# Kernel optimization log

Hardware: AMD Instinct MI355X
Metric: run time of the kernel (lower is better)

Reference implementation:

```python
import jax, jax.numpy as jnp
import numpy as np

D = 1024
H = 16
HD = D // H
S = 2048
B = 2
INNER = 4 * D
EPS = 1e-5


def _layernorm(x, w, b):
    mu = jnp.mean(x, axis=-1, keepdims=True)
    var = jnp.mean(jnp.square(x - mu), axis=-1, keepdims=True)
    return (x - mu) * jax.lax.rsqrt(var + EPS) * w + b


def _rope(x, cos, sin):
    # x: [B, S, H, HD]; cos/sin: [S, HD//2]
    xe, xo = x[..., 0::2], x[..., 1::2]
    c = cos[None, :, None, :]
    s = sin[None, :, None, :]
    oe = xe * c - xo * s
    oo = xe * s + xo * c
    return jnp.stack([oe, oo], axis=-1).reshape(x.shape)


def setup_inputs() -> dict:
    key = jax.random.key(0)
    ks = jax.random.split(key, 12)
    hidden_states = jax.random.normal(ks[0], (B, S, D), dtype=jnp.float32)
    time_step_emb = jax.random.normal(ks[1], (B, 6 * D), dtype=jnp.float32)
    # causal additive mask [1,1,S,S]
    causal = jnp.tril(jnp.ones((S, S), dtype=bool))
    attention_mask = jnp.where(causal, 0.0, -1e9).astype(jnp.float32)[None, None]
    # proper RoPE tables
    inv_freq = 1.0 / (10000.0 ** (np.arange(0, HD, 2, dtype=np.float32) / HD))
    t = np.arange(S, dtype=np.float32)
    freqs = np.outer(t, inv_freq)  # [S, HD//2]
    rope_cos = jnp.asarray(np.cos(freqs))
    rope_sin = jnp.asarray(np.sin(freqs))
    p = 0.02
    params = dict(
        ln1_w=jnp.ones((D,), jnp.float32), ln1_b=jnp.zeros((D,), jnp.float32),
        ln2_w=jnp.ones((D,), jnp.float32), ln2_b=jnp.zeros((D,), jnp.float32),
        c_attn_w=jax.random.normal(ks[2], (D, 3 * D), jnp.float32) * p,
        c_attn_b=jnp.zeros((3 * D,), jnp.float32),
        c_proj_w=jax.random.normal(ks[3], (D, D), jnp.float32) * p,
        c_proj_b=jnp.zeros((D,), jnp.float32),
        fc_w=jax.random.normal(ks[4], (D, INNER), jnp.float32) * p,
        fc_b=jnp.zeros((INNER,), jnp.float32),
        proj_w=jax.random.normal(ks[5], (INNER, D), jnp.float32) * p,
        proj_b=jnp.zeros((D,), jnp.float32),
        scale_shift_table=jax.random.normal(ks[6], (6, D), jnp.float32) / np.sqrt(D),
    )
    return dict(hidden_states=hidden_states, attention_mask=attention_mask,
                time_step_emb=time_step_emb, rope_cos=rope_cos, rope_sin=rope_sin,
                **params)


def reference(hidden_states, attention_mask, time_step_emb, rope_cos, rope_sin,
              ln1_w, ln1_b, ln2_w, ln2_b, c_attn_w, c_attn_b, c_proj_w, c_proj_b,
              fc_w, fc_b, proj_w, proj_b, scale_shift_table):
    b = hidden_states.shape[0]
    mods = scale_shift_table[None] + time_step_emb.reshape(b, 6, D)  # [B,6,D]
    sh_msa, sc_msa, g_msa, sh_mlp, sc_mlp, g_mlp = [mods[:, i:i + 1] for i in range(6)]

    residual = hidden_states
    h = _layernorm(hidden_states, ln1_w, ln1_b) * (1.0 + sc_msa) + sh_msa

    qkv = h @ c_attn_w + c_attn_b  # [B,S,3D]
    q, k, v = jnp.split(qkv, 3, axis=-1)
    q = _rope(q.reshape(b, S, H, HD), rope_cos, rope_sin)
    k = _rope(k.reshape(b, S, H, HD), rope_cos, rope_sin)
    v = v.reshape(b, S, H, HD)
    scores = jnp.einsum('bqhd,bkhd->bhqk', q, k) / np.sqrt(float(HD))
    scores = scores + attention_mask
    attn = jax.nn.softmax(scores, axis=-1)
    out = jnp.einsum('bhqk,bkhd->bqhd', attn, v).reshape(b, S, D)
    attn_out = out @ c_proj_w + c_proj_b

    hidden = attn_out * g_msa + residual
    residual = hidden
    h = _layernorm(hidden, ln2_w, ln2_b) * (1.0 + sc_mlp) + sh_mlp
    h = jax.nn.gelu(h @ fc_w + fc_b, approximate=True)  # gelu_new (tanh approx)
    h = h @ proj_w + proj_b
    return h * g_mlp + residual
```

## Files before the change

### kernel.cpp

```cpp
#include <hip/hip_runtime.h>
#include <hip/hip_bf16.h>

#define D_MODEL 1024
#define N_HEADS 16
#define HEAD_DIM 64
#define SEQ 2048
#define BATCH 2
#define INNER_DIM 4096
#define ROWS (BATCH*SEQ)

using f32x4  = __attribute__((ext_vector_type(4))) float;
using bf16x8 = __attribute__((ext_vector_type(8))) short;

__device__ __forceinline__ void gl_lds16(const void* g, void* l) {
  __builtin_amdgcn_global_load_lds(
      (const __attribute__((address_space(1))) void*)g,
      (__attribute__((address_space(3))) void*)l, 16, 0, 0);
}

__device__ __forceinline__ float bf2f(unsigned short u) {
  union { unsigned int i; float f; } v; v.i = ((unsigned int)u) << 16; return v.f;
}
__device__ __forceinline__ unsigned short f2bf(float f) {
  union { float f; unsigned int i; } v; v.f = f;
  unsigned int x = v.i;
  return (unsigned short)((x + 0x7fffu + ((x >> 16) & 1u)) >> 16);
}

__device__ __forceinline__ float exp2fast(float x) {
  return __builtin_amdgcn_exp2f(x);
}

__device__ __forceinline__ float gelu_tanh(float x) {
  float x3 = x * x * x;
  float z = 0.7978845608028654f * (x + 0.044715f * x3);
  z = fminf(z, 15.0f);
  float e = __expf(2.0f * z);
  float th = (e - 1.0f) / (e + 1.0f);
  return 0.5f * x * (1.0f + th);
}

__global__ void transpose_convert(const float* __restrict__ in,
                                  unsigned short* __restrict__ out,
                                  int K, int N) {
  __shared__ float tile[32][33];
  int n0 = blockIdx.x * 32, k0 = blockIdx.y * 32;
  int tx = threadIdx.x, ty = threadIdx.y;
#pragma unroll
  for (int i = 0; i < 4; i++)
    tile[ty + i * 8][tx] = in[(size_t)(k0 + ty + i * 8) * N + n0 + tx];
  __syncthreads();
#pragma unroll
  for (int i = 0; i < 4; i++)
    out[(size_t)(n0 + ty + i * 8) * K + k0 + tx] = f2bf(tile[tx][ty + i * 8]);
}

template<int SH_IDX, int SC_IDX>
__global__ void ln_mod_kernel(const float* __restrict__ x,
                              const float* __restrict__ lw,
                              const float* __restrict__ lb,
                              const float* __restrict__ sst,
                              const float* __restrict__ temb,
                              unsigned short* __restrict__ out) {
  int row = blockIdx.x;
  int b = row >> 11;
  int t = threadIdx.x;
  const float* xr = x + (size_t)row * D_MODEL;
  float4 v = ((const float4*)xr)[t];
  float s = v.x + v.y + v.z + v.w;
  float s2 = v.x * v.x + v.y * v.y + v.z * v.z + v.w * v.w;
#pragma unroll
  for (int o = 1; o < 64; o <<= 1) { s += __shfl_xor(s, o); s2 += __shfl_xor(s2, o); }
  __shared__ float red[8];
  int wid = t >> 6, lane = t & 63;
  if (lane == 0) { red[wid] = s; red[4 + wid] = s2; }
  __syncthreads();
  s = red[0] + red[1] + red[2] + red[3];
  s2 = red[4] + red[5] + red[6] + red[7];
  float mu = s * (1.0f / D_MODEL);
  float var = s2 * (1.0f / D_MODEL) - mu * mu;
  float rs = rsqrtf(var + 1e-5f);
  int d0 = t * 4;
  float xv[4] = { v.x, v.y, v.z, v.w };
  ushort4 ov;
  unsigned short* po = (unsigned short*)&ov;
#pragma unroll
  for (int j = 0; j < 4; j++) {
    int d = d0 + j;
    float ln = (xv[j] - mu) * rs * lw[d] + lb[d];
    float sc = sst[SC_IDX * D_MODEL + d] + temb[b * 6 * D_MODEL + SC_IDX * D_MODEL + d];
    float sh = sst[SH_IDX * D_MODEL + d] + temb[b * 6 * D_MODEL + SH_IDX * D_MODEL + d];
    po[j] = f2bf(ln * (1.0f + sc) + sh);
  }
  *((ushort4*)(out + (size_t)row * D_MODEL + d0)) = ov;
}

enum { EPI_QKV = 0, EPI_GELU = 2, EPI_PART = 3 };

template<int EPI>
__global__ __launch_bounds__(256, 2)
void gemm64(const unsigned short* __restrict__ A,
            const unsigned short* __restrict__ Bt,
            const float* __restrict__ bias,
            void* C0, void* C1,
            int N, int Ksub, int Kstride,
            const float* __restrict__ cosb,
            const float* __restrict__ sinb) {
  __shared__ unsigned short Alds[2][128 * 64];
  __shared__ unsigned short Blds[2][128 * 64];
  const int t = threadIdx.x;
  const int w = t >> 6, l = t & 63;
  const int lg = l >> 4, ll = l & 15;
  const int wm = w >> 1, wn = w & 1;
  const int kbase = blockIdx.z * Ksub;

  const int nx = gridDim.x;
  const int nwg = nx * gridDim.y;
  const int lid = blockIdx.y * nx + blockIdx.x;
  const int nid = (lid & 7) * (nwg >> 3) + (lid >> 3);
  const int m0 = (nid / nx) * 128, n0 = (nid % nx) * 128;

  void* Cout = blockIdx.z ? C1 : C0;

  f32x4 acc[4][4] = {};

  auto stage = [&](int kt, int buf) {
#pragma unroll
    for (int i = 0; i < 4; i++) {
      int c = i * 256 + t;
      int row = c >> 3, q = c & 7;
      gl_lds16(A + (size_t)(m0 + row) * Kstride + kbase + kt * 64 + ((q ^ (row & 7)) << 3),
               (char*)&Alds[buf][0] + c * 16);
    }
#pragma unroll
    for (int i = 0; i < 4; i++) {
      int c = i * 256 + t;
      int row = c >> 3, q = c & 7;
      gl_lds16(Bt + (size_t)(n0 + row) * Kstride + kbase + kt * 64 + ((q ^ (row & 7)) << 3),
               (char*)&Blds[buf][0] + c * 16);
    }
  };

  stage(0, 0);
  int buf = 0;
  const int nk = Ksub >> 6;
  for (int it = 0; it < nk; ++it) {
    if (it + 1 < nk) {
      stage(it + 1, buf ^ 1);
      asm volatile("s_waitcnt vmcnt(8)" ::: "memory");
    } else {
      asm volatile("s_waitcnt vmcnt(0)" ::: "memory");
    }
    __builtin_amdgcn_s_barrier();
    asm volatile("" ::: "memory");

#pragma unroll
    for (int kk = 0; kk < 2; kk++) {
      bf16x8 af[4], bfr[4];
#pragma unroll
      for (int mf = 0; mf < 4; mf++) {
        int row = wm * 64 + mf * 16 + ll;
        int q = (kk * 4 + lg) ^ (row & 7);
        af[mf] = *(const bf16x8*)(&Alds[buf][0] + row * 64 + q * 8);
      }
#pragma unroll
      for (int nf = 0; nf < 4; nf++) {
        int row = wn * 64 + nf * 16 + ll;
        int q = (kk * 4 + lg) ^ (row & 7);
        bfr[nf] = *(const bf16x8*)(&Blds[buf][0] + row * 64 + q * 8);
      }
#pragma unroll
      for (int mf = 0; mf < 4; mf++)
#pragma unroll
        for (int nf = 0; nf < 4; nf++)
          acc[mf][nf] = __builtin_amdgcn_mfma_f32_16x16x32_bf16(af[mf], bfr[nf], acc[mf][nf], 0, 0, 0);
    }

    asm volatile("" ::: "memory");
    __builtin_amdgcn_s_barrier();
    buf ^= 1;
  }

#pragma unroll
  for (int mf = 0; mf < 4; mf++) {
#pragma unroll
    for (int nf = 0; nf < 4; nf++) {
      int col = n0 + wn * 64 + nf * 16 + ll;
      float bv = (EPI == EPI_PART) ? 0.0f : bias[col];
#pragma unroll
      for (int r = 0; r < 4; r++) {
        int row = m0 + wm * 64 + mf * 16 + lg * 4 + r;
        float v = acc[mf][nf][r] + bv;
        if constexpr (EPI == EPI_QKV) {
          if (col < 2048) {
            float vp = __shfl_xor(v, 1);
            int sp = row & (SEQ - 1);
            int ip = (col & 63) >> 1;
            float cz = cosb[sp * 32 + ip], sz = sinb[sp * 32 + ip];
            float ov = (col & 1) ? (vp * sz + v * cz) : (v * cz - vp * sz);
            if (col < 1024) ov *= 0.18033688011112042f;
            v = ov;
          }
          ((unsigned short*)Cout)[(size_t)row * N + col] = f2bf(v);
        } else if constexpr (EPI == EPI_GELU) {
          ((unsigned short*)Cout)[(size_t)row * N + col] = f2bf(gelu_tanh(v));
        } else {
          ((unsigned short*)Cout)[(size_t)row * N + col] = f2bf(v);
        }
      }
    }
  }
}

__global__ void reduce_gated(const unsigned short* __restrict__ p0,
                             const unsigned short* __restrict__ p1,
                             const float* __restrict__ bias,
                             const float* __restrict__ sst,
                             const float* __restrict__ temb,
                             int g_idx,
                             const float* __restrict__ resid,
                             float* __restrict__ out) {
  int i = blockIdx.x * 256 + threadIdx.x;
  int idx = i * 4;
  int col = idx & 1023;
  int b = idx >> 21;
  ushort4 a0 = *(const ushort4*)(p0 + idx);
  ushort4 a1 = *(const ushort4*)(p1 + idx);
  float4 rv = *(const float4*)(resid + idx);
  float4 o;
  const unsigned short* s0 = (const unsigned short*)&a0;
  const unsigned short* s1 = (const unsigned short*)&a1;
  float* po = (float*)&o;
  const float* pr = (const float*)&rv;
#pragma unroll
  for (int j = 0; j < 4; j++) {
    float s = bf2f(s0[j]) + bf2f(s1[j]) + bias[col + j];
    float g = sst[g_idx * D_MODEL + col + j] + temb[b * 6 * D_MODEL + g_idx * D_MODEL + col + j];
    po[j] = s * g + pr[j];
  }
  *(float4*)(out + idx) = o;
}

__global__ __launch_bounds__(256, 4)
void attn_kernel(const unsigned short* __restrict__ qkv,
                 unsigned short* __restrict__ attn_o) {
  __shared__ unsigned short Klds[2][64 * 64];
  __shared__ unsigned short Vt[2][64 * 64];
  __shared__ unsigned short Plds[4][16 * 64];

  const int id = blockIdx.x;
  const int bh = id & 31;
  const int b = bh >> 4, h = bh & 15;
  const int q0 = (31 - (id >> 5)) * 64;
  const int t = threadIdx.x;
  const int w = t >> 6, l = t & 63;
  const int lg = l >> 4, ll = l & 15;
  const int qw0 = q0 + w * 16;
  const int q_lane = qw0 + ll;

  bf16x8 qf[2];
  {
    const unsigned short* qb = qkv + (size_t)(b * SEQ + q_lane) * 3072 + h * 64;
    qf[0] = *(const bf16x8*)(qb + lg * 8);
    qf[1] = *(const bf16x8*)(qb + 32 + lg * 8);
  }

  const int kp = t & 31, dg = t >> 5;

  f32x4 oacc[4] = {};
  float mrun = -1e30f, lrun = 0.0f;

  {
#pragma unroll
    for (int i = 0; i < 2; i++) {
      int c = i * 256 + t;
      int kr = c >> 3, cc = c & 7;
      gl_lds16(qkv + (size_t)(b * SEQ + kr) * 3072 + 1024 + h * 64 + (cc ^ (kr & 7)) * 8,
               (char*)&Klds[0][0] + c * 16);
    }
    const unsigned short* vp = qkv + (size_t)(b * SEQ + 2 * kp) * 3072 + 2048 + h * 64 + dg * 8;
    union { uint4 u; unsigned short s[8]; } a0, a1;
    a0.u = *(const uint4*)vp;
    a1.u = *(const uint4*)(vp + 3072);
    unsigned int* vt32 = (unsigned int*)&Vt[0][0];
#pragma unroll
    for (int i = 0; i < 8; i++)
      vt32[(dg * 8 + i) * 32 + (((kp >> 2) ^ i) << 2) + (kp & 3)] =
          (unsigned int)a0.s[i] | ((unsigned int)a1.s[i] << 16);
  }
  __syncthreads();

  int buf = 0;
  for (int k0 = 0; k0 <= q0; k0 += 64) {
    const bool has_next = (k0 + 64 <= q0);
    union { uint4 u; unsigned short s[8]; } n0, n1;
    if (has_next) {
#pragma unroll
      for (int i = 0; i < 2; i++) {
        int c = i * 256 + t;
        int kr = c >> 3, cc = c & 7;
        gl_lds16(qkv + (size_t)(b * SEQ + k0 + 64 + kr) * 3072 + 1024 + h * 64 + (cc ^ (kr & 7)) * 8,
                 (char*)&Klds[buf ^ 1][0] + c * 16);
      }
      const unsigned short* vp =
          qkv + (size_t)(b * SEQ + k0 + 64 + 2 * kp) * 3072 + 2048 + h * 64 + dg * 8;
      n0.u = *(const uint4*)vp;
      n1.u = *(const uint4*)(vp + 3072);
    }

    f32x4 s[4] = {};
#pragma unroll
    for (int kk = 0; kk < 2; kk++) {
#pragma unroll
      for (int nf = 0; nf < 4; nf++) {
        int key = nf * 16 + ll;
        int cc = (kk * 4 + lg) ^ (key & 7);
        bf16x8 kf = *(const bf16x8*)((const char*)&Klds[buf][0] + key * 128 + cc * 16);
        s[nf] = __builtin_amdgcn_mfma_f32_16x16x32_bf16(kf, qf[kk], s[nf], 0, 0, 0);
      }
    }
    if (k0 == q0) {
#pragma unroll
      for (int nf = 0; nf < 4; nf++) {
        int key = k0 + nf * 16 + lg * 4;
#pragma unroll
        for (int r = 0; r < 4; r++)
          if (key + r > q_lane) s[nf][r] = -1e30f;
      }
    }
    float mx = -1e30f;
#pragma unroll
    for (int nf = 0; nf < 4; nf++)
#pragma unroll
      for (int r = 0; r < 4; r++) mx = fmaxf(mx, s[nf][r]);
    mx = fmaxf(mx, __shfl_xor(mx, 16));
    mx = fmaxf(mx, __shfl_xor(mx, 32));
    float mnew = fmaxf(mrun, mx);
    float alpha = exp2fast(mrun - mnew);
    mrun = mnew;
    float ps = 0.0f;
#pragma unroll
    for (int nf = 0; nf < 4; nf++)
#pragma unroll
      for (int r = 0; r < 4; r++) {
        float p = exp2fast(s[nf][r] - mnew);
        s[nf][r] = p;
        ps += p;
      }
    ps += __shfl_xor(ps, 16);
    ps += __shfl_xor(ps, 32);
    lrun = lrun * alpha + ps;
#pragma unroll
    for (int nf = 0; nf < 4; nf++)
#pragma unroll
      for (int r = 0; r < 4; r++) oacc[nf][r] *= alpha;

#pragma unroll
    for (int nf = 0; nf < 4; nf++) {
      unsigned int lo = (unsigned int)f2bf(s[nf][0]) | ((unsigned int)f2bf(s[nf][1]) << 16);
      unsigned int hi = (unsigned int)f2bf(s[nf][2]) | ((unsigned int)f2bf(s[nf][3]) << 16);
      int chunk = (nf * 2 + (lg >> 1)) ^ (ll & 7);
      uint2 pv; pv.x = lo; pv.y = hi;
      *(uint2*)((char*)&Plds[w][0] + ll * 128 + chunk * 16 + (lg & 1) * 8) = pv;
    }
    bf16x8 pb[2];
#pragma unroll
    for (int kk = 0; kk < 2; kk++) {
      int pc = (kk * 4 + lg) ^ (ll & 7);
      pb[kk] = *(const bf16x8*)((char*)&Plds[w][0] + ll * 128 + pc * 16);
    }
#pragma unroll
    for (int nf = 0; nf < 4; nf++) {
      int d = nf * 16 + ll;
#pragma unroll
      for (int kk = 0; kk < 2; kk++) {
        int vc = (kk * 4 + lg) ^ (d & 7);
        bf16x8 vb = *(const bf16x8*)((const char*)&Vt[buf][0] + d * 128 + vc * 16);
        oacc[nf] = __builtin_amdgcn_mfma_f32_16x16x32_bf16(vb, pb[kk], oacc[nf], 0, 0, 0);
      }
    }
    if (has_next) {
      unsigned int* vt32 = (unsigned int*)&Vt[buf ^ 1][0];
#pragma unroll
      for (int i = 0; i < 8; i++)
        vt32[(dg * 8 + i) * 32 + (((kp >> 2) ^ i) << 2) + (kp & 3)] =
            (unsigned int)n0.s[i] | ((unsigned int)n1.s[i] << 16);
    }
    __syncthreads();
    buf ^= 1;
  }

  float rl = 1.0f / lrun;
#pragma unroll
  for (int nf = 0; nf < 4; nf++) {
    ushort4 ov;
    ov.x = f2bf(oacc[nf][0] * rl);
    ov.y = f2bf(oacc[nf][1] * rl);
    ov.z = f2bf(oacc[nf][2] * rl);
    ov.w = f2bf(oacc[nf][3] * rl);
    *(ushort4*)(attn_o + (size_t)(b * SEQ + q_lane) * D_MODEL + h * 64 + nf * 16 + lg * 4) = ov;
  }
}

extern "C" void kernel_launch(void* const* d_in, const int* in_sizes, int n_in,
                              void* d_out, int out_size, void* d_ws, size_t ws_size,
                              hipStream_t stream) {
  const float* hidden_states = (const float*)d_in[0];
  const float* temb     = (const float*)d_in[2];
  const float* rope_cos = (const float*)d_in[3];
  const float* rope_sin = (const float*)d_in[4];
  const float* ln1_w    = (const float*)d_in[5];
  const float* ln1_b    = (const float*)d_in[6];
  const float* ln2_w    = (const float*)d_in[7];
  const float* ln2_b    = (const float*)d_in[8];
  const float* c_attn_w = (const float*)d_in[9];
  const float* c_attn_b = (const float*)d_in[10];
  const float* c_proj_w = (const float*)d_in[11];
  const float* c_proj_b = (const float*)d_in[12];
  const float* fc_w     = (const float*)d_in[13];
  const float* fc_b     = (const float*)d_in[14];
  const float* proj_w   = (const float*)d_in[15];
  const float* proj_b   = (const float*)d_in[16];
  const float* sst      = (const float*)d_in[17];

  char* ws = (char*)d_ws;
  unsigned short* wqkv  = (unsigned short*)(ws + 0);
  unsigned short* wproj = (unsigned short*)(ws + 6291456);
  unsigned short* wfc   = (unsigned short*)(ws + 8388608);
  unsigned short* wp2   = (unsigned short*)(ws + 16777216);
  unsigned short* hln   = (unsigned short*)(ws + 25165824);
  unsigned short* qkvb  = (unsigned short*)(ws + 33554432);
  unsigned short* attno = (unsigned short*)(ws + 58720256);
  float*          hidden = (float*)(ws + 67108864);
  unsigned short* rp0 = (unsigned short*)(ws + 33554432);
  unsigned short* rp1 = (unsigned short*)(ws + 41943040);
  unsigned short* h3  = (unsigned short*)(ws + 33554432);
  unsigned short* fp0 = (unsigned short*)(ws + 0);
  unsigned short* fp1 = (unsigned short*)(ws + 8388608);

  dim3 tb(32, 8);
  transpose_convert<<<dim3(3072 / 32, 1024 / 32), tb, 0, stream>>>(c_attn_w, wqkv, 1024, 3072);
  transpose_convert<<<dim3(1024 / 32, 1024 / 32), tb, 0, stream>>>(c_proj_w, wproj, 1024, 1024);
  transpose_convert<<<dim3(4096 / 32, 1024 / 32), tb, 0, stream>>>(fc_w, wfc, 1024, 4096);
  transpose_convert<<<dim3(1024 / 32, 4096 / 32), tb, 0, stream>>>(proj_w, wp2, 4096, 1024);

  ln_mod_kernel<0, 1><<<ROWS, 256, 0, stream>>>(hidden_states, ln1_w, ln1_b, sst, temb, hln);

  gemm64<EPI_QKV><<<dim3(3072 / 128, ROWS / 128, 1), 256, 0, stream>>>(
      hln, wqkv, c_attn_b, qkvb, qkvb, 3072, 1024, 1024, rope_cos, rope_sin);

  attn_kernel<<<dim3(32 * 32), 256, 0, stream>>>(qkvb, attno);

  gemm64<EPI_PART><<<dim3(1024 / 128, ROWS / 128, 2), 256, 0, stream>>>(
      attno, wproj, c_proj_b, rp0, rp1, 1024, 512, 1024, nullptr, nullptr);
  reduce_gated<<<(ROWS * D_MODEL / 4) / 256, 256, 0, stream>>>(
      rp0, rp1, c_proj_b, sst, temb, 2, hidden_states, hidden);

  ln_mod_kernel<3, 4><<<ROWS, 256, 0, stream>>>(hidden, ln2_w, ln2_b, sst, temb, hln);

  gemm64<EPI_GELU><<<dim3(4096 / 128, ROWS / 128, 1), 256, 0, stream>>>(
      hln, wfc, fc_b, h3, h3, 4096, 1024, 1024, nullptr, nullptr);

  gemm64<EPI_PART><<<dim3(1024 / 128, ROWS / 128, 2), 256, 0, stream>>>(
      h3, wp2, proj_b, fp0, fp1, 1024, 2048, 4096, nullptr, nullptr);
  reduce_gated<<<(ROWS * D_MODEL / 4) / 256, 256, 0, stream>>>(
      fp0, fp1, proj_b, sst, temb, 5, hidden, (float*)d_out);
}
```

Measured before the change: 268.6 us.

## Template GEMM on K-tile count with hoisted addresses; fuse reduce with LayerNorm2

The GEMM now takes its K-tile count as a template parameter. Global and LDS addresses are precomputed once, and the main loop is unrolled by two with compile-time buffer indices, which removes per-iteration address arithmetic. Separately, a new reduce_ln kernel fuses the split-K partial reduction, gated residual add and the second LayerNorm/modulation into one pass, dropping a kernel launch and a full read of the hidden tensor. The fused LN uses single-pass E[x^2]-mu^2 variance, which is slightly less numerically robust.

```diff
diff --git a/kernel.cpp b/kernel.cpp
--- a/kernel.cpp
+++ b/kernel.cpp
@@ -1,5 +1,6 @@
 #include <hip/hip_runtime.h>
 #include <hip/hip_bf16.h>
+#include <type_traits>
 
 #define D_MODEL 1024
 #define N_HEADS 16
@@ -97,13 +98,13 @@
 
 enum { EPI_QKV = 0, EPI_GELU = 2, EPI_PART = 3 };
 
-template<int EPI>
+template<int EPI, int NK>
 __global__ __launch_bounds__(256, 2)
 void gemm64(const unsigned short* __restrict__ A,
             const unsigned short* __restrict__ Bt,
             const float* __restrict__ bias,
             void* C0, void* C1,
-            int N, int Ksub, int Kstride,
+            int N, int Kstride,
             const float* __restrict__ cosb,
             const float* __restrict__ sinb) {
   __shared__ unsigned short Alds[2][128 * 64];
@@ -112,7 +113,7 @@
   const int w = t >> 6, l = t & 63;
   const int lg = l >> 4, ll = l & 15;
   const int wm = w >> 1, wn = w & 1;
-  const int kbase = blockIdx.z * Ksub;
+  const int kbase = blockIdx.z * (NK * 64);
 
   const int nx = gridDim.x;
   const int nwg = nx * gridDim.y;
@@ -124,62 +125,80 @@
 
   f32x4 acc[4][4] = {};
 
-  auto stage = [&](int kt, int buf) {
-#pragma unroll
-    for (int i = 0; i < 4; i++) {
-      int c = i * 256 + t;
-      int row = c >> 3, q = c & 7;
-      gl_lds16(A + (size_t)(m0 + row) * Kstride + kbase + kt * 64 + ((q ^ (row & 7)) << 3),
-               (char*)&Alds[buf][0] + c * 16);
-    }
-#pragma unroll
-    for (int i = 0; i < 4; i++) {
-      int c = i * 256 + t;
-      int row = c >> 3, q = c & 7;
-      gl_lds16(Bt + (size_t)(n0 + row) * Kstride + kbase + kt * 64 + ((q ^ (row & 7)) << 3),
-               (char*)&Blds[buf][0] + c * 16);
-    }
-  };
-
-  stage(0, 0);
-  int buf = 0;
-  const int nk = Ksub >> 6;
-  for (int it = 0; it < nk; ++it) {
-    if (it + 1 < nk) {
-      stage(it + 1, buf ^ 1);
+  const unsigned short* ga[4];
+  const unsigned short* gb[4];
+#pragma unroll
+  for (int i = 0; i < 4; i++) {
+    int c = i * 256 + t, row = c >> 3, q = c & 7;
+    ga[i] = A + (size_t)(m0 + row) * Kstride + kbase + ((q ^ (row & 7)) << 3);
+    gb[i] = Bt + (size_t)(n0 + row) * Kstride + kbase + ((q ^ (row & 7)) << 3);
+  }
+  const unsigned short* ra[4][2];
+  const unsigned short* rb[4][2];
+#pragma unroll
+  for (int f = 0; f < 4; f++) {
+    int rowA = wm * 64 + f * 16 + ll;
+    int rowB = wn * 64 + f * 16 + ll;
+#pragma unroll
+    for (int kk = 0; kk < 2; kk++) {
+      ra[f][kk] = &Alds[0][rowA * 64 + ((((kk * 4 + lg) ^ (rowA & 7))) << 3)];
+      rb[f][kk] = &Blds[0][rowB * 64 + ((((kk * 4 + lg) ^ (rowB & 7))) << 3)];
+    }
+  }
+
+#pragma unroll
+  for (int i = 0; i < 4; i++) {
+    gl_lds16(ga[i], (char*)&Alds[0][0] + (i * 256 + t) * 16); ga[i] += 64;
+  }
+#pragma unroll
+  for (int i = 0; i < 4; i++) {
+    gl_lds16(gb[i], (char*)&Blds[0][0] + (i * 256 + t) * 16); gb[i] += 64;
+  }
+
+  auto giter = [&](auto BUFC, bool last) {
+    constexpr int BUF = decltype(BUFC)::value;
+    constexpr int NBUF = BUF ^ 1;
+    if (!last) {
+#pragma unroll
+      for (int i = 0; i < 4; i++) {
+        gl_lds16(ga[i], (char*)&Alds[NBUF][0] + (i * 256 + t) * 16); ga[i] += 64;
+      }
+#pragma unroll
+      for (int i = 0; i < 4; i++) {
+        gl_lds16(gb[i], (char*)&Blds[NBUF][0] + (i * 256 + t) * 16); gb[i] += 64;
+      }
       asm volatile("s_waitcnt vmcnt(8)" ::: "memory");
     } else {
       asm volatile("s_waitcnt vmcnt(0)" ::: "memory");
     }
     __builtin_amdgcn_s_barrier();
     asm volatile("" ::: "memory");
-
 #pragma unroll
     for (int kk = 0; kk < 2; kk++) {
       bf16x8 af[4], bfr[4];
 #pragma unroll
-      for (int mf = 0; mf < 4; mf++) {
-        int row = wm * 64 + mf * 16 + ll;
-        int q = (kk * 4 + lg) ^ (row & 7);
-        af[mf] = *(const bf16x8*)(&Alds[buf][0] + row * 64 + q * 8);
-      }
-#pragma unroll
-      for (int nf = 0; nf < 4; nf++) {
-        int row = wn * 64 + nf * 16 + ll;
-        int q = (kk * 4 + lg) ^ (row & 7);
-        bfr[nf] = *(const bf16x8*)(&Blds[buf][0] + row * 64 + q * 8);
-      }
+      for (int mf = 0; mf < 4; mf++)
+        af[mf] = *(const bf16x8*)(ra[mf][kk] + BUF * 8192);
+#pragma unroll
+      for (int nf = 0; nf < 4; nf++)
+        bfr[nf] = *(const bf16x8*)(rb[nf][kk] + BUF * 8192);
 #pragma unroll
       for (int mf = 0; mf < 4; mf++)
 #pragma unroll
         for (int nf = 0; nf < 4; nf++)
           acc[mf][nf] = __builtin_amdgcn_mfma_f32_16x16x32_bf16(af[mf], bfr[nf], acc[mf][nf], 0, 0, 0);
     }
-
     asm volatile("" ::: "memory");
     __builtin_amdgcn_s_barrier();
-    buf ^= 1;
-  }
+  };
+
+#pragma unroll 1
+  for (int u = 0; u < NK - 2; u += 2) {
+    giter(std::integral_constant<int, 0>{}, false);
+    giter(std::integral_constant<int, 1>{}, false);
+  }
+  giter(std::integral_constant<int, 0>{}, false);
+  giter(std::integral_constant<int, 1>{}, true);
 
 #pragma unroll
   for (int mf = 0; mf < 4; mf++) {
@@ -210,6 +229,60 @@
       }
     }
   }
+}
+
+__global__ void reduce_ln(const unsigned short* __restrict__ p0,
+                          const unsigned short* __restrict__ p1,
+                          const float* __restrict__ bias,
+                          const float* __restrict__ sst,
+                          const float* __restrict__ temb,
+                          const float* __restrict__ resid,
+                          float* __restrict__ hidden,
+                          const float* __restrict__ lw,
+                          const float* __restrict__ lb,
+                          unsigned short* __restrict__ hln) {
+  int row = blockIdx.x, b = row >> 11, t = threadIdx.x;
+  size_t base = (size_t)row * D_MODEL + t * 4;
+  int col = t * 4;
+  ushort4 a0 = *(const ushort4*)(p0 + base);
+  ushort4 a1 = *(const ushort4*)(p1 + base);
+  float4 rv = *(const float4*)(resid + base);
+  const unsigned short* s0 = (const unsigned short*)&a0;
+  const unsigned short* s1 = (const unsigned short*)&a1;
+  const float* pr = (const float*)&rv;
+  float h[4];
+  float s = 0.0f, s2 = 0.0f;
+#pragma unroll
+  for (int j = 0; j < 4; j++) {
+    int d = col + j;
+    float g = sst[2 * D_MODEL + d] + temb[b * 6 * D_MODEL + 2 * D_MODEL + d];
+    float v = (bf2f(s0[j]) + bf2f(s1[j]) + bias[d]) * g + pr[j];
+    h[j] = v; s += v; s2 += v * v;
+  }
+  float4 hv; hv.x = h[0]; hv.y = h[1]; hv.z = h[2]; hv.w = h[3];
+  *(float4*)(hidden + base) = hv;
+#pragma unroll
+  for (int o = 1; o < 64; o <<= 1) { s += __shfl_xor(s, o); s2 += __shfl_xor(s2, o); }
+  __shared__ float red[8];
+  int wid = t >> 6, lane = t & 63;
+  if (lane == 0) { red[wid] = s; red[4 + wid] = s2; }
+  __syncthreads();
+  s = red[0] + red[1] + red[2] + red[3];
+  s2 = red[4] + red[5] + red[6] + red[7];
+  float mu = s * (1.0f / D_MODEL);
+  float var = s2 * (1.0f / D_MODEL) - mu * mu;
+  float rs = rsqrtf(var + 1e-5f);
+  ushort4 ov;
+  unsigned short* po = (unsigned short*)&ov;
+#pragma unroll
+  for (int j = 0; j < 4; j++) {
+    int d = col + j;
+    float ln = (h[j] - mu) * rs * lw[d] + lb[d];
+    float sc = sst[4 * D_MODEL + d] + temb[b * 6 * D_MODEL + 4 * D_MODEL + d];
+    float sh = sst[3 * D_MODEL + d] + temb[b * 6 * D_MODEL + 3 * D_MODEL + d];
+    po[j] = f2bf(ln * (1.0f + sc) + sh);
+  }
+  *(ushort4*)(hln + base) = ov;
 }
 
 __global__ void reduce_gated(const unsigned short* __restrict__ p0,
@@ -446,23 +519,21 @@
 
   ln_mod_kernel<0, 1><<<ROWS, 256, 0, stream>>>(hidden_states, ln1_w, ln1_b, sst, temb, hln);
 
-  gemm64<EPI_QKV><<<dim3(3072 / 128, ROWS / 128, 1), 256, 0, stream>>>(
-      hln, wqkv, c_attn_b, qkvb, qkvb, 3072, 1024, 1024, rope_cos, rope_sin);
+  gemm64<EPI_QKV, 16><<<dim3(3072 / 128, ROWS / 128, 1), 256, 0, stream>>>(
+      hln, wqkv, c_attn_b, qkvb, qkvb, 3072, 1024, rope_cos, rope_sin);
 
   attn_kernel<<<dim3(32 * 32), 256, 0, stream>>>(qkvb, attno);
 
-  gemm64<EPI_PART><<<dim3(1024 / 128, ROWS / 128, 2), 256, 0, stream>>>(
-      attno, wproj, c_proj_b, rp0, rp1, 1024, 512, 1024, nullptr, nullptr);
-  reduce_gated<<<(ROWS * D_MODEL / 4) / 256, 256, 0, stream>>>(
-      rp0, rp1, c_proj_b, sst, temb, 2, hidden_states, hidden);
-
-  ln_mod_kernel<3, 4><<<ROWS, 256, 0, stream>>>(hidden, ln2_w, ln2_b, sst, temb, hln);
-
-  gemm64<EPI_GELU><<<dim3(4096 / 128, ROWS / 128, 1), 256, 0, stream>>>(
-      hln, wfc, fc_b, h3, h3, 4096, 1024, 1024, nullptr, nullptr);
-
-  gemm64<EPI_PART><<<dim3(1024 / 128, ROWS / 128, 2), 256, 0, stream>>>(
-      h3, wp2, proj_b, fp0, fp1, 1024, 2048, 4096, nullptr, nullptr);
+  gemm64<EPI_PART, 8><<<dim3(1024 / 128, ROWS / 128, 2), 256, 0, stream>>>(
+      attno, wproj, c_proj_b, rp0, rp1, 1024, 1024, nullptr, nullptr);
+  reduce_ln<<<ROWS, 256, 0, stream>>>(
+      rp0, rp1, c_proj_b, sst, temb, hidden_states, hidden, ln2_w, ln2_b, hln);
+
+  gemm64<EPI_GELU, 16><<<dim3(4096 / 128, ROWS / 128, 1), 256, 0, stream>>>(
+      hln, wfc, fc_b, h3, h3, 4096, 1024, nullptr, nullptr);
+
+  gemm64<EPI_PART, 32><<<dim3(1024 / 128, ROWS / 128, 2), 256, 0, stream>>>(
+      h3, wp2, proj_b, fp0, fp1, 1024, 4096, nullptr, nullptr);
   reduce_gated<<<(ROWS * D_MODEL / 4) / 256, 256, 0, stream>>>(
       fp0, fp1, proj_b, sst, temb, 5, hidden, (float*)d_out);
 }
```

Measured after the change: 254.2 us. -5.4%, faster.
